# Optimization experiments

Measured on AMD Instinct MI355X. Metric: run time of the kernel, lower is better.

Reference implementation:

```python
import jax, jax.numpy as jnp
import numpy as np

DET_SIZE = 5120
DET_THRESHOLD = 0.5
NMS_THRESHOLD = 0.4
STRIDES = (8, 16, 32)
NUM_ANCHORS = 2
TOP_K = 2048  # fixed pre-NMS candidate count (jit-friendly stand-in for torch.where filtering)


def _anchor_centers(stride):
    n = DET_SIZE // stride
    g = jnp.arange(n, dtype=jnp.float32) * stride
    X, Y = jnp.meshgrid(g, g, indexing='xy')       # matches torch.meshgrid(..., indexing='xy')
    c = jnp.stack([X, Y], axis=-1).reshape(-1, 2)  # (n*n, 2), x fastest
    return jnp.repeat(c, NUM_ANCHORS, axis=0)      # stack([c]*2, dim=1).reshape(-1,2) == interleaved repeat


def _pairwise_iou(b):
    # b: (K,4) xyxy
    area = jnp.clip(b[:, 2] - b[:, 0], 0.0) * jnp.clip(b[:, 3] - b[:, 1], 0.0)
    lt = jnp.maximum(b[:, None, :2], b[None, :, :2])
    rb = jnp.minimum(b[:, None, 2:], b[None, :, 2:])
    wh = jnp.clip(rb - lt, 0.0)
    inter = wh[..., 0] * wh[..., 1]
    return inter / (area[:, None] + area[None, :] - inter + 1e-9)


def _forward(scores8, bbox8, lms8, scores16, bbox16, lms16, scores32, bbox32, lms32, det_scale):
    confs, boxes, lmss = [], [], []
    per_stride = [(scores8, bbox8, lms8), (scores16, bbox16, lms16), (scores32, bbox32, lms32)]
    for (conf, bbox, lms), stride in zip(per_stride, STRIDES):
        c = _anchor_centers(stride)                 # (N,2)
        b = bbox * stride                            # distance-style offsets scaled by stride
        l = lms * stride
        box = jnp.concatenate([c - b[:, :2], c + b[:, 2:4]], axis=-1) / det_scale  # (N,4) xyxy
        pts = (c[:, None, :] + l.reshape(-1, 5, 2)) / det_scale                    # (N,5,2)
        confs.append(conf.reshape(-1)); boxes.append(box); lmss.append(pts)
    conf = jnp.concatenate(confs)
    box = jnp.concatenate(boxes, axis=0)
    pts = jnp.concatenate(lmss, axis=0)
    # score threshold via masking (fixed shapes); below-threshold entries get conf=-1
    conf_m = jnp.where(conf >= DET_THRESHOLD, conf, -1.0)
    top_conf, top_idx = jax.lax.top_k(conf_m, TOP_K)
    top_box = box[top_idx]          # (K,4)
    top_pts = pts[top_idx]          # (K,5,2)
    valid = top_conf >= DET_THRESHOLD
    iou = _pairwise_iou(top_box)    # (K,K)
    later = jnp.arange(TOP_K)
    def body(i, keep):
        supp = (iou[i] > NMS_THRESHOLD) & (later > i) & keep[i] & valid[i]
        return keep & ~supp
    keep = jax.lax.fori_loop(0, TOP_K, body, valid)  # greedy NMS in descending-score order
    m = keep.astype(top_box.dtype)
    # (K, 15) = [conf | bbox(4) | lms(10)], suppressed/invalid rows zeroed
    return jnp.concatenate([(top_conf * m)[:, None], top_box * m[:, None], top_pts.reshape(TOP_K, 10) * m[:, None]], axis=-1)


def setup_inputs() -> dict:
    key = jax.random.key(0)
    ks = jax.random.split(key, 9)
    inp = {}
    for i, s in enumerate(STRIDES):
        n = DET_SIZE // s
        N = n * n * NUM_ANCHORS
        inp[f'scores{s}'] = jax.random.uniform(ks[3 * i], (N,), dtype=jnp.float32)
        inp[f'bbox{s}'] = jax.random.uniform(ks[3 * i + 1], (N, 4), dtype=jnp.float32) * 8.0
        inp[f'lms{s}'] = jax.random.normal(ks[3 * i + 2], (N, 10), dtype=jnp.float32) * 4.0
    inp['det_scale'] = jnp.array(0.5, dtype=jnp.float32)
    return inp


def reference(scores8, bbox8, lms8, scores16, bbox16, lms16, scores32, bbox32, lms32, det_scale):
    return _forward(scores8, bbox8, lms8, scores16, bbox16, lms16, scores32, bbox32, lms32, det_scale)
```

## Files before the change

kernel.cpp:

```cpp
#include <hip/hip_runtime.h>
#include <stdint.h>
#include <stddef.h>

#pragma clang fp contract(off)

#define N8   819200u
#define N16  204800u
#define N32  51200u
#define NTOT 1075200u
#define TOPK 2048
#define CAND_MAX 8192
#define NBIN 8192u
#define BINSHIFT 10
#define NMS_THR 0.4f
#define DET_THR 0.5f

#define OFF_HIST   0u
#define OFF_META   32768u
#define OFF_CAND   32832u
#define OFF_TIDX   98368u
#define OFF_TCONF  106560u
#define OFF_BOX    114752u
#define OFF_DIAGT  147520u
#define OFF_SUPPT  155968u

__device__ __forceinline__ float load_conf(unsigned a, const float* __restrict__ s8,
                                           const float* __restrict__ s16,
                                           const float* __restrict__ s32) {
  if (a < N8) return s8[a];
  if (a < N8 + N16) return s16[a - N8];
  return s32[a - (N8 + N16)];
}

__device__ __forceinline__ void decode(unsigned a,
    const float* __restrict__ b8, const float* __restrict__ l8,
    const float* __restrict__ b16, const float* __restrict__ l16,
    const float* __restrict__ b32, const float* __restrict__ l32,
    float& cx, float& cy, float& s, const float*& bb, const float*& lm) {
  if (a < N8) {
    unsigned cell = a >> 1;
    cx = (float)((cell % 640u) * 8u); cy = (float)((cell / 640u) * 8u);
    s = 8.f; bb = b8 + (size_t)a * 4; lm = l8 + (size_t)a * 10;
  } else if (a < N8 + N16) {
    unsigned loc = a - N8; unsigned cell = loc >> 1;
    cx = (float)((cell % 320u) * 16u); cy = (float)((cell / 320u) * 16u);
    s = 16.f; bb = b16 + (size_t)loc * 4; lm = l16 + (size_t)loc * 10;
  } else {
    unsigned loc = a - (N8 + N16); unsigned cell = loc >> 1;
    cx = (float)((cell % 160u) * 32u); cy = (float)((cell / 160u) * 32u);
    s = 32.f; bb = b32 + (size_t)loc * 4; lm = l32 + (size_t)loc * 10;
  }
}

__global__ void k_hist(const float* __restrict__ s8, const float* __restrict__ s16,
                       const float* __restrict__ s32, unsigned* __restrict__ hist) {
  unsigned i = blockIdx.x * blockDim.x + threadIdx.x;
  unsigned st = gridDim.x * blockDim.x;
  for (unsigned a = i; a < NTOT; a += st) {
    float c = load_conf(a, s8, s16, s32);
    if (c >= DET_THR) {
      unsigned v = (__float_as_uint(c) - 0x3F000000u) >> BINSHIFT;
      if (v > NBIN - 1u) v = NBIN - 1u;
      atomicAdd(&hist[v], 1u);
    }
  }
}

__global__ void __launch_bounds__(1024) k_scan(const unsigned* __restrict__ hist,
                                               unsigned* __restrict__ meta) {
  __shared__ unsigned suf[1024];
  int t = threadIdx.x;
  const unsigned* hp = hist + (size_t)t * 8;
  unsigned s = 0;
  for (int b = 0; b < 8; b++) s += hp[b];
  suf[t] = s;
  __syncthreads();
  for (int d = 1; d < 1024; d <<= 1) {
    unsigned v = (t + d < 1024) ? suf[t + d] : 0u;
    __syncthreads();
    suf[t] += v;
    __syncthreads();
  }
  unsigned total = suf[0];
  unsigned mine = suf[t];
  unsigned nxt = (t < 1023) ? suf[t + 1] : 0u;
  if (total < (unsigned)TOPK) {
    if (t == 0) { meta[0] = 0u; meta[2] = total; }
    return;
  }
  if (mine >= (unsigned)TOPK && nxt < (unsigned)TOPK) {
    unsigned run = nxt, cut = (unsigned)t * 8u;
    for (int b = 7; b >= 0; b--) {
      run += hp[b];
      if (run >= (unsigned)TOPK) { cut = (unsigned)t * 8u + (unsigned)b; break; }
    }
    meta[0] = cut; meta[2] = total;
  }
}

__global__ void k_compact(const float* __restrict__ s8, const float* __restrict__ s16,
                          const float* __restrict__ s32, unsigned* __restrict__ meta,
                          unsigned long long* __restrict__ cand) {
  unsigned cut = meta[0];
  unsigned i = blockIdx.x * blockDim.x + threadIdx.x;
  unsigned st = gridDim.x * blockDim.x;
  for (unsigned a = i; a < NTOT; a += st) {
    float c = load_conf(a, s8, s16, s32);
    if (c >= DET_THR) {
      unsigned b = __float_as_uint(c);
      unsigned v = (b - 0x3F000000u) >> BINSHIFT;
      if (v >= cut) {
        unsigned pos = atomicAdd(&meta[3], 1u);
        if (pos < (unsigned)CAND_MAX)
          cand[pos] = ((unsigned long long)b << 32) |
                      (unsigned long long)(0xFFFFFFFFu - a);
      }
    }
  }
}

__global__ void __launch_bounds__(256) k_rank(
    const unsigned long long* __restrict__ cand, const unsigned* __restrict__ meta,
    const float* __restrict__ b8, const float* __restrict__ l8,
    const float* __restrict__ b16, const float* __restrict__ l16,
    const float* __restrict__ b32, const float* __restrict__ l32,
    const float* __restrict__ dsp,
    unsigned* __restrict__ tidx, float* __restrict__ tconf, float* __restrict__ box) {
  unsigned count = meta[3];
  if (count > (unsigned)CAND_MAX) count = (unsigned)CAND_MAX;
  unsigned wave = blockIdx.x * 4u + (threadIdx.x >> 6);
  unsigned lane = threadIdx.x & 63u;
  if (wave >= count) return;
  unsigned long long my = cand[wave];
  unsigned cnt = 0;
  for (unsigned i = lane; i < count; i += 64u)
    cnt += (cand[i] > my) ? 1u : 0u;
  for (int d = 32; d > 0; d >>= 1) cnt += __shfl_down(cnt, d);
  if (lane == 0 && cnt < (unsigned)TOPK) {
    unsigned r = cnt;
    unsigned a = 0xFFFFFFFFu - (unsigned)(my & 0xFFFFFFFFull);
    float conf = __uint_as_float((unsigned)(my >> 32));
    float cx, cy, s; const float* bb; const float* lm;
    decode(a, b8, l8, b16, l16, b32, l32, cx, cy, s, bb, lm);
    float ds = dsp[0];
    float b0 = bb[0] * s, b1 = bb[1] * s, b2 = bb[2] * s, b3 = bb[3] * s;
    box[r * 4 + 0] = (cx - b0) / ds;
    box[r * 4 + 1] = (cy - b1) / ds;
    box[r * 4 + 2] = (cx + b2) / ds;
    box[r * 4 + 3] = (cy + b3) / ds;
    tidx[r] = a; tconf[r] = conf;
  }
}

__global__ void __launch_bounds__(256) k_supp(const float* __restrict__ box,
                                              unsigned* __restrict__ supp_t,
                                              unsigned* __restrict__ diagT) {
  int i = blockIdx.x;
  const float4 bi = ((const float4*)box)[i];
  float ai = fmaxf(bi.z - bi.x, 0.f) * fmaxf(bi.w - bi.y, 0.f);
  int tid = threadIdx.x;
  int lane = tid & 63, wv = tid >> 6;
  int c = i >> 5, k = i & 31;
  for (int base = 0; base < TOPK; base += 256) {
    int j = base + tid;
    const float4 bj = ((const float4*)box)[j];
    float aj = fmaxf(bj.z - bj.x, 0.f) * fmaxf(bj.w - bj.y, 0.f);
    float ltx = fmaxf(bi.x, bj.x), lty = fmaxf(bi.y, bj.y);
    float rbx = fminf(bi.z, bj.z), rby = fminf(bi.w, bj.w);
    float w = fmaxf(rbx - ltx, 0.f), h = fmaxf(rby - lty, 0.f);
    float inter = w * h;
    float iou = inter / (ai + aj - inter + 1e-9f);
    bool pred = (iou > NMS_THR) && (j > i);
    unsigned long long word = __ballot(pred);
    int w64 = (base >> 6) + wv;
    if (lane == 0) {
      supp_t[c * 2048 + (2 * w64) * 32 + k]     = (unsigned)(word & 0xFFFFFFFFull);
      supp_t[c * 2048 + (2 * w64 + 1) * 32 + k] = (unsigned)(word >> 32);
      if (w64 == (i >> 6))
        diagT[k * 64 + c] = (unsigned)(word >> (((i >> 5) & 1) * 32));
    }
  }
}

__global__ void __launch_bounds__(256) k_nms_out(
    const unsigned* __restrict__ supp_t, const unsigned* __restrict__ diagT,
    const unsigned* __restrict__ meta,
    const unsigned* __restrict__ tidx, const float* __restrict__ tconf,
    const float* __restrict__ b8, const float* __restrict__ l8,
    const float* __restrict__ b16, const float* __restrict__ l16,
    const float* __restrict__ b32, const float* __restrict__ l32,
    const float* __restrict__ dsp, float* __restrict__ out) {
  __shared__ unsigned keepw[64];
  int tid = threadIdx.x;
  if (tid < 64) {
    int lane = tid;
    unsigned count = meta[3];
    if (count > (unsigned)TOPK) count = (unsigned)TOPK;
    unsigned lo = (unsigned)lane * 32u;
    unsigned kw = (count >= lo + 32u) ? 0xFFFFFFFFu
                : (count <= lo ? 0u : ((1u << (count - lo)) - 1u));
    const uint4* rp4 = (const uint4*)supp_t + (size_t)lane * 8;
    uint4 T0[8], T1[8], T2[8], T3[8];
    unsigned dg[32];

#define LOADT(BUF, C)                                                         \
  _Pragma("unroll") for (int q = 0; q < 8; q++)                               \
      BUF[q] = rp4[(size_t)(unsigned)((C) * 512 + q)];

#pragma unroll
    for (int k = 0; k < 32; k++) dg[k] = diagT[k * 64 + lane];
    LOADT(T0, 0) LOADT(T1, 1) LOADT(T2, 2) LOADT(T3, 3)

#define STEP(BUF, CC)                                                         \
  {                                                                           \
    int cc = (CC);                                                            \
    unsigned w = __builtin_amdgcn_readlane(kw, cc);                           \
    _Pragma("unroll") for (int k = 0; k < 32; k++) {                          \
      unsigned d = __builtin_amdgcn_readlane(dg[k], cc);                      \
      w &= ~(((w >> k) & 1u) ? d : 0u);                                       \
    }                                                                         \
    unsigned acc0 = 0u, acc1 = 0u, acc2 = 0u, acc3 = 0u;                      \
    _Pragma("unroll") for (int q = 0; q < 8; q++) {                           \
      unsigned m0 = (unsigned)((int)(w << (31 - (4 * q + 0))) >> 31);         \
      unsigned m1 = (unsigned)((int)(w << (31 - (4 * q + 1))) >> 31);         \
      unsigned m2 = (unsigned)((int)(w << (31 - (4 * q + 2))) >> 31);         \
      unsigned m3 = (unsigned)((int)(w << (31 - (4 * q + 3))) >> 31);         \
      acc0 |= BUF[q].x & m0;                                                  \
      acc1 |= BUF[q].y & m1;                                                  \
      acc2 |= BUF[q].z & m2;                                                  \
      acc3 |= BUF[q].w & m3;                                                  \
    }                                                                         \
    kw &= ~((acc0 | acc1) | (acc2 | acc3));                                   \
    if (cc + 4 < 64) { LOADT(BUF, cc + 4) }                                   \
  }

#pragma unroll 1
    for (int c = 0; c < 64; c += 4) {
      STEP(T0, c + 0)
      STEP(T1, c + 1)
      STEP(T2, c + 2)
      STEP(T3, c + 3)
    }
#undef LOADT
#undef STEP
    keepw[lane] = kw;
  }
  __syncthreads();
  float ds = dsp[0];
  for (int r = tid; r < TOPK; r += 256) {
    bool kept = (keepw[r >> 5] >> (r & 31)) & 1u;
    float o[15];
    if (kept) {
      unsigned a = tidx[r];
      float cx, cy, s; const float* bb; const float* lm;
      decode(a, b8, l8, b16, l16, b32, l32, cx, cy, s, bb, lm);
      o[0] = tconf[r];
      float b0 = bb[0] * s, b1 = bb[1] * s, b2 = bb[2] * s, b3 = bb[3] * s;
      o[1] = (cx - b0) / ds;
      o[2] = (cy - b1) / ds;
      o[3] = (cx + b2) / ds;
      o[4] = (cy + b3) / ds;
      for (int p = 0; p < 5; p++) {
        float lx = lm[2 * p] * s, ly = lm[2 * p + 1] * s;
        o[5 + 2 * p] = (cx + lx) / ds;
        o[6 + 2 * p] = (cy + ly) / ds;
      }
    } else {
      for (int cc = 0; cc < 15; cc++) o[cc] = 0.f;
    }
    for (int cc = 0; cc < 15; cc++) out[(size_t)r * 15 + cc] = o[cc];
  }
}

extern "C" void kernel_launch(void* const* d_in, const int* in_sizes, int n_in,
                              void* d_out, int out_size, void* d_ws, size_t ws_size,
                              hipStream_t stream) {
  const float* s8  = (const float*)d_in[0];
  const float* b8  = (const float*)d_in[1];
  const float* l8  = (const float*)d_in[2];
  const float* s16 = (const float*)d_in[3];
  const float* b16 = (const float*)d_in[4];
  const float* l16 = (const float*)d_in[5];
  const float* s32 = (const float*)d_in[6];
  const float* b32 = (const float*)d_in[7];
  const float* l32 = (const float*)d_in[8];
  const float* dsp = (const float*)d_in[9];
  char* ws = (char*)d_ws;
  unsigned* hist = (unsigned*)(ws + OFF_HIST);
  unsigned* meta = (unsigned*)(ws + OFF_META);
  unsigned long long* cand = (unsigned long long*)(ws + OFF_CAND);
  unsigned* tidx = (unsigned*)(ws + OFF_TIDX);
  float* tconf = (float*)(ws + OFF_TCONF);
  float* box = (float*)(ws + OFF_BOX);
  unsigned* diagT = (unsigned*)(ws + OFF_DIAGT);
  unsigned* supp_t = (unsigned*)(ws + OFF_SUPPT);
  float* out = (float*)d_out;

  hipMemsetAsync(ws, 0, OFF_META + 64, stream);
  k_hist<<<2048, 256, 0, stream>>>(s8, s16, s32, hist);
  k_scan<<<1, 1024, 0, stream>>>(hist, meta);
  k_compact<<<2048, 256, 0, stream>>>(s8, s16, s32, meta, cand);
  k_rank<<<CAND_MAX / 4, 256, 0, stream>>>(cand, meta, b8, l8, b16, l16, b32, l32,
                                           dsp, tidx, tconf, box);
  k_supp<<<TOPK, 256, 0, stream>>>(box, supp_t, diagT);
  k_nms_out<<<1, 256, 0, stream>>>(supp_t, diagT, meta, tidx, tconf,
                                   b8, l8, b16, l16, b32, l32, dsp, out);
}
```

Measured before the change: 127.9 us.

## Spread greedy NMS suppression reduction across eight waves with new bitmask layout

The suppression bitmask is now written as 64-bit words in a chunk-row-major layout, and the single-wave NMS loop becomes a 512-thread block. Wave 0 resolves each 32-candidate chunk serially using the diagonal masks. All eight waves then OR the suppression rows of the kept candidates into per-lane accumulators and publish the next chunk's accumulated mask through shared memory. The goal is to spread the per-chunk OR reduction and global loads across more waves, at the cost of two block barriers per chunk (128 in total) on the serial critical path.

```diff
diff --git a/kernel.cpp b/kernel.cpp
--- a/kernel.cpp
+++ b/kernel.cpp
@@ -153,7 +153,7 @@
 }
 
 __global__ void __launch_bounds__(256) k_supp(const float* __restrict__ box,
-                                              unsigned* __restrict__ supp_t,
+                                              unsigned long long* __restrict__ supp64,
                                               unsigned* __restrict__ diagT) {
   int i = blockIdx.x;
   const float4 bi = ((const float4*)box)[i];
@@ -174,15 +174,14 @@
     unsigned long long word = __ballot(pred);
     int w64 = (base >> 6) + wv;
     if (lane == 0) {
-      supp_t[c * 2048 + (2 * w64) * 32 + k]     = (unsigned)(word & 0xFFFFFFFFull);
-      supp_t[c * 2048 + (2 * w64 + 1) * 32 + k] = (unsigned)(word >> 32);
+      supp64[(size_t)c * 1024 + k * 32 + w64] = word;
       if (w64 == (i >> 6))
         diagT[k * 64 + c] = (unsigned)(word >> (((i >> 5) & 1) * 32));
     }
   }
 }
 
-__global__ void __launch_bounds__(256) k_nms_out(
+__global__ void __launch_bounds__(512) k_nms_out(
     const unsigned* __restrict__ supp_t, const unsigned* __restrict__ diagT,
     const unsigned* __restrict__ meta,
     const unsigned* __restrict__ tidx, const float* __restrict__ tconf,
@@ -191,70 +190,83 @@
     const float* __restrict__ b32, const float* __restrict__ l32,
     const float* __restrict__ dsp, float* __restrict__ out) {
   __shared__ unsigned keepw[64];
+  __shared__ unsigned wacc[8];
   int tid = threadIdx.x;
-  if (tid < 64) {
-    int lane = tid;
-    unsigned count = meta[3];
-    if (count > (unsigned)TOPK) count = (unsigned)TOPK;
-    unsigned lo = (unsigned)lane * 32u;
-    unsigned kw = (count >= lo + 32u) ? 0xFFFFFFFFu
-                : (count <= lo ? 0u : ((1u << (count - lo)) - 1u));
-    const uint4* rp4 = (const uint4*)supp_t + (size_t)lane * 8;
-    uint4 T0[8], T1[8], T2[8], T3[8];
-    unsigned dg[32];
-
-#define LOADT(BUF, C)                                                         \
-  _Pragma("unroll") for (int q = 0; q < 8; q++)                               \
-      BUF[q] = rp4[(size_t)(unsigned)((C) * 512 + q)];
-
+  int v = tid >> 6, l = tid & 63;
+  unsigned count = meta[3];
+  if (count > (unsigned)TOPK) count = (unsigned)TOPK;
+  if (tid < 8) wacc[tid] = 0u;
+  unsigned dg[32];
+  if (v == 0) {
 #pragma unroll
-    for (int k = 0; k < 32; k++) dg[k] = diagT[k * 64 + lane];
-    LOADT(T0, 0) LOADT(T1, 1) LOADT(T2, 2) LOADT(T3, 3)
-
-#define STEP(BUF, CC)                                                         \
+    for (int k = 0; k < 32; k++) dg[k] = diagT[k * 64 + l];
+  }
+  int r = v * 4 + (l >> 4);
+  int g = l & 15;
+  const uint4* bp = (const uint4*)supp_t + ((size_t)r * 16 + g);
+  uint4 P0 = bp[0 * 512], P1 = bp[1 * 512], P2 = bp[2 * 512], P3 = bp[3 * 512];
+  uint4 A; A.x = 0u; A.y = 0u; A.z = 0u; A.w = 0u;
+  __syncthreads();
+
+#define STEP(PP, CC)                                                          \
   {                                                                           \
-    int cc = (CC);                                                            \
-    unsigned w = __builtin_amdgcn_readlane(kw, cc);                           \
-    _Pragma("unroll") for (int k = 0; k < 32; k++) {                          \
-      unsigned d = __builtin_amdgcn_readlane(dg[k], cc);                      \
-      w &= ~(((w >> k) & 1u) ? d : 0u);                                       \
+    const int ch = (CC);                                                      \
+    if (v == 0) {                                                             \
+      unsigned app = (l < 8) ? wacc[l] : 0u;                                  \
+      app |= __shfl_xor(app, 1);                                              \
+      app |= __shfl_xor(app, 2);                                              \
+      app |= __shfl_xor(app, 4);                                              \
+      unsigned appl = __builtin_amdgcn_readlane(app, 0);                      \
+      unsigned lo = (unsigned)ch * 32u;                                       \
+      unsigned init = (count >= lo + 32u) ? 0xFFFFFFFFu                       \
+                    : (count <= lo ? 0u : ((1u << (count - lo)) - 1u));       \
+      unsigned w = init & ~appl;                                              \
+      _Pragma("unroll") for (int k = 0; k < 32; k++) {                        \
+        unsigned d = __builtin_amdgcn_readlane(dg[k], ch);                    \
+        w &= ~(((w >> k) & 1u) ? d : 0u);                                     \
+      }                                                                       \
+      if (l == 0) keepw[ch] = w;                                              \
     }                                                                         \
-    unsigned acc0 = 0u, acc1 = 0u, acc2 = 0u, acc3 = 0u;                      \
-    _Pragma("unroll") for (int q = 0; q < 8; q++) {                           \
-      unsigned m0 = (unsigned)((int)(w << (31 - (4 * q + 0))) >> 31);         \
-      unsigned m1 = (unsigned)((int)(w << (31 - (4 * q + 1))) >> 31);         \
-      unsigned m2 = (unsigned)((int)(w << (31 - (4 * q + 2))) >> 31);         \
-      unsigned m3 = (unsigned)((int)(w << (31 - (4 * q + 3))) >> 31);         \
-      acc0 |= BUF[q].x & m0;                                                  \
-      acc1 |= BUF[q].y & m1;                                                  \
-      acc2 |= BUF[q].z & m2;                                                  \
-      acc3 |= BUF[q].w & m3;                                                  \
+    __syncthreads();                                                          \
+    unsigned wc = keepw[ch];                                                  \
+    unsigned m = 0u - ((wc >> r) & 1u);                                       \
+    unsigned x0 = PP.x & m, x1 = PP.y & m, x2 = PP.z & m, x3 = PP.w & m;      \
+    x0 |= __shfl_xor(x0, 16); x1 |= __shfl_xor(x1, 16);                       \
+    x2 |= __shfl_xor(x2, 16); x3 |= __shfl_xor(x3, 16);                       \
+    x0 |= __shfl_xor(x0, 32); x1 |= __shfl_xor(x1, 32);                       \
+    x2 |= __shfl_xor(x2, 32); x3 |= __shfl_xor(x3, 32);                       \
+    A.x |= x0; A.y |= x1; A.z |= x2; A.w |= x3;                               \
+    if (ch + 4 < 64) PP = bp[(size_t)(ch + 4) * 512];                         \
+    {                                                                         \
+      const int nc = ch + 1;                                                  \
+      if (nc < 64 && g == (nc >> 2) && (l >> 4) == 0) {                       \
+        const int sel = nc & 3;                                               \
+        unsigned comp = (sel == 0) ? A.x : (sel == 1) ? A.y                   \
+                       : (sel == 2) ? A.z : A.w;                              \
+        wacc[v] = comp;                                                       \
+      }                                                                       \
     }                                                                         \
-    kw &= ~((acc0 | acc1) | (acc2 | acc3));                                   \
-    if (cc + 4 < 64) { LOADT(BUF, cc + 4) }                                   \
+    __syncthreads();                                                          \
   }
 
 #pragma unroll 1
-    for (int c = 0; c < 64; c += 4) {
-      STEP(T0, c + 0)
-      STEP(T1, c + 1)
-      STEP(T2, c + 2)
-      STEP(T3, c + 3)
-    }
-#undef LOADT
+  for (int c = 0; c < 64; c += 4) {
+    STEP(P0, c + 0)
+    STEP(P1, c + 1)
+    STEP(P2, c + 2)
+    STEP(P3, c + 3)
+  }
 #undef STEP
-    keepw[lane] = kw;
-  }
-  __syncthreads();
+
   float ds = dsp[0];
-  for (int r = tid; r < TOPK; r += 256) {
-    bool kept = (keepw[r >> 5] >> (r & 31)) & 1u;
+  for (int rr = tid; rr < TOPK; rr += 512) {
+    bool kept = (keepw[rr >> 5] >> (rr & 31)) & 1u;
     float o[15];
     if (kept) {
-      unsigned a = tidx[r];
+      unsigned a = tidx[rr];
       float cx, cy, s; const float* bb; const float* lm;
       decode(a, b8, l8, b16, l16, b32, l32, cx, cy, s, bb, lm);
-      o[0] = tconf[r];
+      o[0] = tconf[rr];
       float b0 = bb[0] * s, b1 = bb[1] * s, b2 = bb[2] * s, b3 = bb[3] * s;
       o[1] = (cx - b0) / ds;
       o[2] = (cy - b1) / ds;
@@ -268,7 +280,7 @@
     } else {
       for (int cc = 0; cc < 15; cc++) o[cc] = 0.f;
     }
-    for (int cc = 0; cc < 15; cc++) out[(size_t)r * 15 + cc] = o[cc];
+    for (int cc = 0; cc < 15; cc++) out[(size_t)rr * 15 + cc] = o[cc];
   }
 }
 
@@ -302,7 +314,7 @@
   k_compact<<<2048, 256, 0, stream>>>(s8, s16, s32, meta, cand);
   k_rank<<<CAND_MAX / 4, 256, 0, stream>>>(cand, meta, b8, l8, b16, l16, b32, l32,
                                            dsp, tidx, tconf, box);
-  k_supp<<<TOPK, 256, 0, stream>>>(box, supp_t, diagT);
-  k_nms_out<<<1, 256, 0, stream>>>(supp_t, diagT, meta, tidx, tconf,
+  k_supp<<<TOPK, 256, 0, stream>>>(box, (unsigned long long*)supp_t, diagT);
+  k_nms_out<<<1, 512, 0, stream>>>(supp_t, diagT, meta, tidx, tconf,
                                    b8, l8, b16, l16, b32, l32, dsp, out);
 }
```

Measured after the change: 138.4 us. +8.2%, slower.

## Re-layout suppression matrix for 64-bit ballot stores and coalesced NMS loads

Applied to the files above, without the earlier changes.

The suppression-bitmask matrix is rearranged so that k_supp writes each 64-bit ballot word with a single nontemporal store instead of two scattered 32-bit stores. The single-wave greedy NMS kernel changes to match: each lane now reads 32 scalar words strided by 64 (coalesced across lanes) rather than 8 uint4 vectors per lane. The aim is to cut store transactions in the producer and improve load coalescing in the serial NMS loop. The cost is more load instructions per chunk and more registers in the NMS kernel, which now sets launch bounds with a minimum of one block.

```diff
diff --git a/kernel.cpp b/kernel.cpp
--- a/kernel.cpp
+++ b/kernel.cpp
@@ -153,7 +153,7 @@
 }
 
 __global__ void __launch_bounds__(256) k_supp(const float* __restrict__ box,
-                                              unsigned* __restrict__ supp_t,
+                                              unsigned long long* __restrict__ supp64,
                                               unsigned* __restrict__ diagT) {
   int i = blockIdx.x;
   const float4 bi = ((const float4*)box)[i];
@@ -174,15 +174,15 @@
     unsigned long long word = __ballot(pred);
     int w64 = (base >> 6) + wv;
     if (lane == 0) {
-      supp_t[c * 2048 + (2 * w64) * 32 + k]     = (unsigned)(word & 0xFFFFFFFFull);
-      supp_t[c * 2048 + (2 * w64 + 1) * 32 + k] = (unsigned)(word >> 32);
+      __builtin_nontemporal_store(word, &supp64[(size_t)c * 1024 + k * 32 + w64]);
       if (w64 == (i >> 6))
-        diagT[k * 64 + c] = (unsigned)(word >> (((i >> 5) & 1) * 32));
-    }
-  }
-}
-
-__global__ void __launch_bounds__(256) k_nms_out(
+        __builtin_nontemporal_store(
+            (unsigned)(word >> (((i >> 5) & 1) * 32)), &diagT[k * 64 + c]);
+    }
+  }
+}
+
+__global__ void __launch_bounds__(256, 1) k_nms_out(
     const unsigned* __restrict__ supp_t, const unsigned* __restrict__ diagT,
     const unsigned* __restrict__ meta,
     const unsigned* __restrict__ tidx, const float* __restrict__ tconf,
@@ -193,30 +193,30 @@
   __shared__ unsigned keepw[64];
   int tid = threadIdx.x;
   if (tid < 64) {
-    int lane = tid;
+    int l = tid;
     unsigned count = meta[3];
     if (count > (unsigned)TOPK) count = (unsigned)TOPK;
-    unsigned lo = (unsigned)lane * 32u;
+    unsigned lo = (unsigned)l * 32u;
     unsigned kw = (count >= lo + 32u) ? 0xFFFFFFFFu
                 : (count <= lo ? 0u : ((1u << (count - lo)) - 1u));
-    const uint4* rp4 = (const uint4*)supp_t + (size_t)lane * 8;
-    uint4 T0[8], T1[8], T2[8], T3[8];
+    const unsigned* sp = supp_t + l;
     unsigned dg[32];
-
-#define LOADT(BUF, C)                                                         \
-  _Pragma("unroll") for (int q = 0; q < 8; q++)                               \
-      BUF[q] = rp4[(size_t)(unsigned)((C) * 512 + q)];
-
 #pragma unroll
-    for (int k = 0; k < 32; k++) dg[k] = diagT[k * 64 + lane];
+    for (int k = 0; k < 32; k++) dg[k] = diagT[k * 64 + l];
+    unsigned T0[32], T1[32], T2[32], T3[32];
+
+#define LOADT(BUF, CH)                                                        \
+  _Pragma("unroll") for (int k = 0; k < 32; k++)                              \
+      BUF[k] = sp[(size_t)(unsigned)((CH) * 2048 + k * 64)];
+
     LOADT(T0, 0) LOADT(T1, 1) LOADT(T2, 2) LOADT(T3, 3)
 
 #define STEP(BUF, CC)                                                         \
   {                                                                           \
-    int cc = (CC);                                                            \
-    unsigned w = __builtin_amdgcn_readlane(kw, cc);                           \
+    const int ch = (CC);                                                      \
+    unsigned w = __builtin_amdgcn_readlane(kw, ch);                           \
     _Pragma("unroll") for (int k = 0; k < 32; k++) {                          \
-      unsigned d = __builtin_amdgcn_readlane(dg[k], cc);                      \
+      unsigned d = __builtin_amdgcn_readlane(dg[k], ch);                      \
       w &= ~(((w >> k) & 1u) ? d : 0u);                                       \
     }                                                                         \
     unsigned acc0 = 0u, acc1 = 0u, acc2 = 0u, acc3 = 0u;                      \
@@ -225,13 +225,13 @@
       unsigned m1 = (unsigned)((int)(w << (31 - (4 * q + 1))) >> 31);         \
       unsigned m2 = (unsigned)((int)(w << (31 - (4 * q + 2))) >> 31);         \
       unsigned m3 = (unsigned)((int)(w << (31 - (4 * q + 3))) >> 31);         \
-      acc0 |= BUF[q].x & m0;                                                  \
-      acc1 |= BUF[q].y & m1;                                                  \
-      acc2 |= BUF[q].z & m2;                                                  \
-      acc3 |= BUF[q].w & m3;                                                  \
+      acc0 |= BUF[4 * q + 0] & m0;                                            \
+      acc1 |= BUF[4 * q + 1] & m1;                                            \
+      acc2 |= BUF[4 * q + 2] & m2;                                            \
+      acc3 |= BUF[4 * q + 3] & m3;                                            \
     }                                                                         \
     kw &= ~((acc0 | acc1) | (acc2 | acc3));                                   \
-    if (cc + 4 < 64) { LOADT(BUF, cc + 4) }                                   \
+    if (ch + 4 < 64) { LOADT(BUF, ch + 4) }                                   \
   }
 
 #pragma unroll 1
@@ -243,18 +243,18 @@
     }
 #undef LOADT
 #undef STEP
-    keepw[lane] = kw;
+    keepw[l] = kw;
   }
   __syncthreads();
   float ds = dsp[0];
-  for (int r = tid; r < TOPK; r += 256) {
-    bool kept = (keepw[r >> 5] >> (r & 31)) & 1u;
+  for (int rr = tid; rr < TOPK; rr += 256) {
+    bool kept = (keepw[rr >> 5] >> (rr & 31)) & 1u;
     float o[15];
     if (kept) {
-      unsigned a = tidx[r];
+      unsigned a = tidx[rr];
       float cx, cy, s; const float* bb; const float* lm;
       decode(a, b8, l8, b16, l16, b32, l32, cx, cy, s, bb, lm);
-      o[0] = tconf[r];
+      o[0] = tconf[rr];
       float b0 = bb[0] * s, b1 = bb[1] * s, b2 = bb[2] * s, b3 = bb[3] * s;
       o[1] = (cx - b0) / ds;
       o[2] = (cy - b1) / ds;
@@ -268,7 +268,7 @@
     } else {
       for (int cc = 0; cc < 15; cc++) o[cc] = 0.f;
     }
-    for (int cc = 0; cc < 15; cc++) out[(size_t)r * 15 + cc] = o[cc];
+    for (int cc = 0; cc < 15; cc++) out[(size_t)rr * 15 + cc] = o[cc];
   }
 }
 
@@ -302,7 +302,7 @@
   k_compact<<<2048, 256, 0, stream>>>(s8, s16, s32, meta, cand);
   k_rank<<<CAND_MAX / 4, 256, 0, stream>>>(cand, meta, b8, l8, b16, l16, b32, l32,
                                            dsp, tidx, tconf, box);
-  k_supp<<<TOPK, 256, 0, stream>>>(box, supp_t, diagT);
+  k_supp<<<TOPK, 256, 0, stream>>>(box, (unsigned long long*)supp_t, diagT);
   k_nms_out<<<1, 256, 0, stream>>>(supp_t, diagT, meta, tidx, tconf,
                                    b8, l8, b16, l16, b32, l32, dsp, out);
 }
```

Result: slower. 130.5 us (+2.0%).
